# Kernel optimization log

Hardware: AMD Instinct MI355X
Metric: run time of the kernel (lower is better)

The kernel has to match this reference:

```python
import jax, jax.numpy as jnp
import numpy as np

D = 768
H = 12
HD = 64
S = 77
FF = 3072
EPS = 1e-5


def _layernorm(x, w, b):
    mu = jnp.mean(x, axis=-1, keepdims=True)
    var = jnp.mean(jnp.square(x - mu), axis=-1, keepdims=True)
    return (x - mu) * jax.lax.rsqrt(var + EPS) * w + b


def setup_inputs() -> dict:
    key = jax.random.key(0)
    ks = jax.random.split(key, 18)
    s = 1.0 / np.sqrt(D)
    sf = 1.0 / np.sqrt(FF)
    return {
        "x": jax.random.normal(ks[0], (512, S, D), dtype=jnp.float32),
        "ln1_w": jnp.ones((D,), jnp.float32),
        "ln1_b": jnp.zeros((D,), jnp.float32),
        "qw": jax.random.uniform(ks[1], (D, D), jnp.float32, -s, s),
        "qb": jax.random.uniform(ks[2], (D,), jnp.float32, -s, s),
        "kw": jax.random.uniform(ks[3], (D, D), jnp.float32, -s, s),
        "kb": jax.random.uniform(ks[4], (D,), jnp.float32, -s, s),
        "vw": jax.random.uniform(ks[5], (D, D), jnp.float32, -s, s),
        "vb": jax.random.uniform(ks[6], (D,), jnp.float32, -s, s),
        "ow": jax.random.uniform(ks[7], (D, D), jnp.float32, -s, s),
        "ob": jax.random.uniform(ks[8], (D,), jnp.float32, -s, s),
        "ln2_w": jnp.ones((D,), jnp.float32),
        "ln2_b": jnp.zeros((D,), jnp.float32),
        "fc1_w": jax.random.uniform(ks[9], (FF, D), jnp.float32, -s, s),
        "fc1_b": jax.random.uniform(ks[10], (FF,), jnp.float32, -s, s),
        "fc2_w": jax.random.uniform(ks[11], (D, FF), jnp.float32, -sf, sf),
        "fc2_b": jax.random.uniform(ks[12], (D,), jnp.float32, -sf, sf),
    }


def reference(x, ln1_w, ln1_b, qw, qb, kw, kb, vw, vb, ow, ob,
              ln2_w, ln2_b, fc1_w, fc1_b, fc2_w, fc2_b):
    B = x.shape[0]
    # --- attention block ---
    h = _layernorm(x, ln1_w, ln1_b)
    q = (h @ qw.T + qb) * 0.125
    k = h @ kw.T + kb
    v = h @ vw.T + vb
    # [B, S, H, HD] -> [B, H, S, HD]
    q = q.reshape(B, S, H, HD).transpose(0, 2, 1, 3)
    k = k.reshape(B, S, H, HD).transpose(0, 2, 1, 3)
    v = v.reshape(B, S, H, HD).transpose(0, 2, 1, 3)
    scores = jnp.einsum('bhqd,bhkd->bhqk', q, k)  # [B,H,S,S]
    # causal additive mask: -inf strictly above diagonal
    mask = jnp.triu(jnp.full((S, S), -jnp.inf, dtype=scores.dtype), 1)
    scores = scores + mask
    attn = jax.nn.softmax(scores, axis=-1)
    ctx = jnp.einsum('bhqk,bhkd->bhqd', attn, v)  # [B,H,S,HD]
    ctx = ctx.transpose(0, 2, 1, 3).reshape(B, S, D)
    x = x + (ctx @ ow.T + ob)
    # --- MLP block with QuickGELU ---
    res = x
    h2 = _layernorm(x, ln2_w, ln2_b) @ fc1_w.T + fc1_b
    h2 = h2 * jax.nn.sigmoid(h2 * 1.702)
    return res + (h2 @ fc2_w.T + fc2_b)
```

## Files before the change

kernel.cpp:

```cpp
#include <hip/hip_runtime.h>

typedef unsigned short u16;
typedef __bf16 v8bf __attribute__((ext_vector_type(8)));
typedef unsigned short u16x8 __attribute__((ext_vector_type(8)));
typedef float v4f __attribute__((ext_vector_type(4)));

#define DEV __device__ __forceinline__

constexpr int M_TOK = 512 * 77;

DEV u16 f2bf(float f) {
  union { float f; unsigned int u; } v; v.f = f;
  unsigned int r = v.u + 0x7fffu + ((v.u >> 16) & 1u);
  return (u16)(r >> 16);
}

DEV void gload16(const void* g, void* l) {
  __builtin_amdgcn_global_load_lds((const __attribute__((address_space(1))) void*)g,
                                   (__attribute__((address_space(3))) void*)l, 16, 0, 0);
}

__global__ void cvt4_k(const float* __restrict__ src, u16* __restrict__ dst, int n4, float scale) {
  int i = blockIdx.x * blockDim.x + threadIdx.x;
  if (i >= n4) return;
  const float4 v = ((const float4*)src)[i];
  ushort4 o;
  o.x = f2bf(v.x * scale); o.y = f2bf(v.y * scale);
  o.z = f2bf(v.z * scale); o.w = f2bf(v.w * scale);
  ((ushort4*)dst)[i] = o;
}

__global__ void qkvb_k(const float* __restrict__ qb, const float* __restrict__ kb,
                       const float* __restrict__ vb, float* __restrict__ dst) {
  int i = blockIdx.x * 256 + threadIdx.x;
  if (i >= 2304) return;
  dst[i] = (i < 768) ? qb[i] * 0.125f : (i < 1536 ? kb[i - 768] : vb[i - 1536]);
}

__global__ __launch_bounds__(256) void ln_k(const float* __restrict__ x, const float* __restrict__ w,
                                            const float* __restrict__ bvec, u16* __restrict__ out, int nrows) {
  const int lane = threadIdx.x & 63;
  const int row = blockIdx.x * 4 + (threadIdx.x >> 6);
  if (row >= nrows) return;
  const float4* xr = (const float4*)(x + (size_t)row * 768);
  float4 v[3];
  float sum = 0.f, sq = 0.f;
#pragma unroll
  for (int t = 0; t < 3; ++t) {
    v[t] = xr[lane + 64 * t];
    sum += v[t].x + v[t].y + v[t].z + v[t].w;
    sq  += v[t].x * v[t].x + v[t].y * v[t].y + v[t].z * v[t].z + v[t].w * v[t].w;
  }
#pragma unroll
  for (int o = 1; o < 64; o <<= 1) { sum += __shfl_xor(sum, o, 64); sq += __shfl_xor(sq, o, 64); }
  const float mean = sum * (1.f / 768.f);
  const float inv = rsqrtf(sq * (1.f / 768.f) - mean * mean + 1e-5f);
  u16* orow = out + (size_t)row * 768;
#pragma unroll
  for (int t = 0; t < 3; ++t) {
    const int c = 4 * (lane + 64 * t);
    ushort4 o4;
    o4.x = f2bf((v[t].x - mean) * inv * w[c + 0] + bvec[c + 0]);
    o4.y = f2bf((v[t].y - mean) * inv * w[c + 1] + bvec[c + 1]);
    o4.z = f2bf((v[t].z - mean) * inv * w[c + 2] + bvec[c + 2]);
    o4.w = f2bf((v[t].w - mean) * inv * w[c + 3] + bvec[c + 3]);
    *(ushort4*)(orow + c) = o4;
  }
}

template <int OUTF32, int ACT, int RES>
__global__ __launch_bounds__(256, 2) void gemm_k(
    const u16* __restrict__ A, const u16* __restrict__ Bw,
    const float* __restrict__ bias, const float* __restrict__ res,
    void* __restrict__ out, int M, int N, int K) {
  __shared__ u16 sA[2][128 * 32];
  __shared__ u16 sB[2][128 * 32];
  const int tid = threadIdx.x;
  const int lane = tid & 63;
  const int wv = tid >> 6;
  const int wr = wv >> 1, wc = wv & 1;
  const int m0 = blockIdx.y * 128, n0 = blockIdx.x * 128;
  const int frow = lane & 15, fk = (lane >> 4) * 8;

  v4f acc[4][4];
#pragma unroll
  for (int i = 0; i < 4; ++i)
#pragma unroll
    for (int j = 0; j < 4; ++j) acc[i][j] = (v4f){0.f, 0.f, 0.f, 0.f};

  const int srow = tid >> 2;
  const int skc = (tid & 3) * 8;
  const size_t aBase0 = (size_t)(m0 + srow) * K + skc;
  const size_t aBase1 = (size_t)(m0 + 64 + srow) * K + skc;
  const size_t bBase0 = (size_t)(n0 + srow) * K + skc;
  const size_t bBase1 = (size_t)(n0 + 64 + srow) * K + skc;
  const int ldsOff0 = (tid & ~63) * 8;

  auto stage = [&](int buf, int kt) {
    const int kb = kt * 32;
    gload16(A + aBase0 + kb, &sA[buf][ldsOff0]);
    gload16(A + aBase1 + kb, &sA[buf][2048 + ldsOff0]);
    gload16(Bw + bBase0 + kb, &sB[buf][ldsOff0]);
    gload16(Bw + bBase1 + kb, &sB[buf][2048 + ldsOff0]);
  };

  const int KT = K >> 5;
  stage(0, 0);
  __syncthreads();
  for (int kt = 0; kt < KT; ++kt) {
    const int cur = kt & 1;
    if (kt + 1 < KT) stage(cur ^ 1, kt + 1);
    v8bf fa[4], fb[4];
#pragma unroll
    for (int i = 0; i < 4; ++i)
      fa[i] = *(const v8bf*)&sA[cur][(wr * 64 + i * 16 + frow) * 32 + fk];
#pragma unroll
    for (int j = 0; j < 4; ++j)
      fb[j] = *(const v8bf*)&sB[cur][(wc * 64 + j * 16 + frow) * 32 + fk];
#pragma unroll
    for (int i = 0; i < 4; ++i)
#pragma unroll
      for (int j = 0; j < 4; ++j)
        acc[i][j] = __builtin_amdgcn_mfma_f32_16x16x32_bf16(fa[i], fb[j], acc[i][j], 0, 0, 0);
    __syncthreads();
  }

#pragma unroll
  for (int i = 0; i < 4; ++i) {
    const int rowb = m0 + wr * 64 + i * 16 + (lane >> 4) * 4;
#pragma unroll
    for (int j = 0; j < 4; ++j) {
      const int col = n0 + wc * 64 + j * 16 + (lane & 15);
      const float bv = bias[col];
#pragma unroll
      for (int r = 0; r < 4; ++r) {
        float v = acc[i][j][r] + bv;
        if (ACT) v = v * (1.f / (1.f + __expf(-1.702f * v)));
        const size_t off = (size_t)(rowb + r) * N + col;
        if (RES) v += res[off];
        if (OUTF32) ((float*)out)[off] = v;
        else ((u16*)out)[off] = f2bf(v);
      }
    }
  }
}

__global__ __launch_bounds__(256) void attn_k(const u16* __restrict__ qkv, u16* __restrict__ ctx) {
  __shared__ u16 sQK[10240];
  __shared__ u16 sVt[64 * 120];
  __shared__ float sS[80][81];
  const int tid = threadIdx.x;
  const int lane = tid & 63;
  const int wv = tid >> 6;
  const int b = blockIdx.x / 12;
  const int h = blockIdx.x % 12;
  u16* sQ = sQK;
  u16* sK = sQK + 5120;
  u16* sP = sQK;

  for (int i = tid; i < 10240 + 64 * 120; i += 256) {
    if (i < 10240) sQK[i] = 0; else sVt[i - 10240] = 0;
  }
  __syncthreads();

  const size_t tokBase = (size_t)(b * 77) * 2304 + h * 64;
  for (int c = tid; c < 77 * 8; c += 256) {
    const int row = c >> 3, k8 = (c & 7) * 8;
    const size_t src = tokBase + (size_t)row * 2304 + k8;
    *(u16x8*)&sQ[row * 64 + k8] = *(const u16x8*)&qkv[src];
    *(u16x8*)&sK[row * 64 + k8] = *(const u16x8*)&qkv[src + 768];
    u16x8 v = *(const u16x8*)&qkv[src + 1536];
#pragma unroll
    for (int j = 0; j < 8; ++j) sVt[(k8 + j) * 120 + row] = v[j];
  }
  __syncthreads();

  const int frow = lane & 15, fk = (lane >> 4) * 8;
  for (int t = wv; t < 25; t += 4) {
    const int it = t / 5, jt = t % 5;
    v4f acc = {0.f, 0.f, 0.f, 0.f};
#pragma unroll
    for (int kk = 0; kk < 2; ++kk) {
      v8bf a = *(const v8bf*)&sQ[(it * 16 + frow) * 64 + kk * 32 + fk];
      v8bf bb = *(const v8bf*)&sK[(jt * 16 + frow) * 64 + kk * 32 + fk];
      acc = __builtin_amdgcn_mfma_f32_16x16x32_bf16(a, bb, acc, 0, 0, 0);
    }
    const int col = jt * 16 + frow;
#pragma unroll
    for (int r = 0; r < 4; ++r) {
      const int row = it * 16 + (lane >> 4) * 4 + r;
      sS[row][col] = (col > row) ? -1e30f : acc[r];
    }
  }
  __syncthreads();

  if (tid < 80) {
    const int row = tid;
    float mx = -1e30f;
    for (int c2 = 0; c2 < 80; ++c2) mx = fmaxf(mx, sS[row][c2]);
    float sum = 0.f;
    for (int c2 = 0; c2 < 80; ++c2) { float e = __expf(sS[row][c2] - mx); sum += e; sS[row][c2] = e; }
    const float inv = 1.f / sum;
    for (int c2 = 0; c2 < 80; ++c2) sP[row * 96 + c2] = f2bf(sS[row][c2] * inv);
    for (int c2 = 80; c2 < 96; ++c2) sP[row * 96 + c2] = 0;
  }
  __syncthreads();

  const size_t outBase = (size_t)(b * 77) * 768 + h * 64;
  for (int t = wv; t < 20; t += 4) {
    const int it = t / 4, jt = t % 4;
    v4f acc = {0.f, 0.f, 0.f, 0.f};
#pragma unroll
    for (int kk = 0; kk < 3; ++kk) {
      v8bf a = *(const v8bf*)&sP[(it * 16 + frow) * 96 + kk * 32 + fk];
      v8bf bb = *(const v8bf*)&sVt[(jt * 16 + frow) * 120 + kk * 32 + fk];
      acc = __builtin_amdgcn_mfma_f32_16x16x32_bf16(a, bb, acc, 0, 0, 0);
    }
    const int col = jt * 16 + frow;
#pragma unroll
    for (int r = 0; r < 4; ++r) {
      const int row = it * 16 + (lane >> 4) * 4 + r;
      if (row < 77) ctx[outBase + (size_t)row * 768 + col] = f2bf(acc[r]);
    }
  }
}

extern "C" void kernel_launch(void* const* d_in, const int* in_sizes, int n_in,
                              void* d_out, int out_size, void* d_ws, size_t ws_size,
                              hipStream_t stream) {
  const float* x    = (const float*)d_in[0];
  const float* ln1w = (const float*)d_in[1];
  const float* ln1b = (const float*)d_in[2];
  const float* qw   = (const float*)d_in[3];
  const float* qb   = (const float*)d_in[4];
  const float* kw   = (const float*)d_in[5];
  const float* kb   = (const float*)d_in[6];
  const float* vw   = (const float*)d_in[7];
  const float* vb   = (const float*)d_in[8];
  const float* ow   = (const float*)d_in[9];
  const float* ob   = (const float*)d_in[10];
  const float* ln2w = (const float*)d_in[11];
  const float* ln2b = (const float*)d_in[12];
  const float* f1wf = (const float*)d_in[13];
  const float* f1b  = (const float*)d_in[14];
  const float* f2wf = (const float*)d_in[15];
  const float* f2b  = (const float*)d_in[16];
  float* outp = (float*)d_out;

  char* p = (char*)d_ws;
  auto alloc = [&](size_t bytes) { char* r = p; p += (bytes + 255) & ~(size_t)255; return r; };
  u16* wqkv = (u16*)alloc((size_t)2304 * 768 * 2);
  u16* owb  = (u16*)alloc((size_t)768 * 768 * 2);
  u16* f1w  = (u16*)alloc((size_t)3072 * 768 * 2);
  u16* f2w  = (u16*)alloc((size_t)768 * 3072 * 2);
  float* qkvb = (float*)alloc(2304 * 4);
  u16* bufA = (u16*)alloc((size_t)M_TOK * 768 * 2);
  u16* bufB = (u16*)alloc((size_t)M_TOK * 3072 * 2);

  cvt4_k<<<576, 256, 0, stream>>>(qw, wqkv, 147456, 0.125f);
  cvt4_k<<<576, 256, 0, stream>>>(kw, wqkv + 589824, 147456, 1.f);
  cvt4_k<<<576, 256, 0, stream>>>(vw, wqkv + 1179648, 147456, 1.f);
  cvt4_k<<<576, 256, 0, stream>>>(ow, owb, 147456, 1.f);
  cvt4_k<<<2304, 256, 0, stream>>>(f1wf, f1w, 589824, 1.f);
  cvt4_k<<<2304, 256, 0, stream>>>(f2wf, f2w, 589824, 1.f);
  qkvb_k<<<9, 256, 0, stream>>>(qb, kb, vb, qkvb);

  ln_k<<<M_TOK / 4, 256, 0, stream>>>(x, ln1w, ln1b, bufA, M_TOK);
  gemm_k<0, 0, 0><<<dim3(18, 308), 256, 0, stream>>>(bufA, wqkv, qkvb, nullptr, bufB, M_TOK, 2304, 768);
  attn_k<<<512 * 12, 256, 0, stream>>>(bufB, bufA);
  gemm_k<1, 0, 1><<<dim3(6, 308), 256, 0, stream>>>(bufA, owb, ob, x, outp, M_TOK, 768, 768);
  ln_k<<<M_TOK / 4, 256, 0, stream>>>(outp, ln2w, ln2b, bufA, M_TOK);
  gemm_k<0, 1, 0><<<dim3(24, 308), 256, 0, stream>>>(bufA, f1w, f1b, nullptr, bufB, M_TOK, 3072, 768);
  gemm_k<1, 0, 1><<<dim3(6, 308), 256, 0, stream>>>(bufB, f2w, f2b, outp, outp, M_TOK, 768, 3072);
}
```

Before: 1.083 ms.

## Replace 128x128 GEMM with 256x256 8-wave tile, 4-stage pipeline, XCD swizzle

Replaces the 128x128, 4-wave, double-buffered GEMM with a 256x256 tile run by 8 waves. It adds a 4-deep global-to-LDS pipeline with explicit vmcnt waits and barriers, an XOR-swizzled LDS layout to avoid bank conflicts, s_setprio around the MFMA bursts, and a workgroup remap that groups tiles per XCD for L2 locality. The goal is higher arithmetic intensity, fewer stalls on global loads, and better cache reuse. The costs are heavier register and LDS use (128KB of LDS per block), far fewer blocks, and dependence on M and N dividing by 256, which holds here (39424 = 154*256).

```diff
diff --git a/kernel.cpp b/kernel.cpp
--- a/kernel.cpp
+++ b/kernel.cpp
@@ -18,6 +18,10 @@
 DEV void gload16(const void* g, void* l) {
   __builtin_amdgcn_global_load_lds((const __attribute__((address_space(1))) void*)g,
                                    (__attribute__((address_space(3))) void*)l, 16, 0, 0);
+}
+
+DEV v4f MF(v8bf a, v8bf b, v4f c) {
+  return __builtin_amdgcn_mfma_f32_16x16x32_bf16(a, b, c, 0, 0, 0);
 }
 
 __global__ void cvt4_k(const float* __restrict__ src, u16* __restrict__ dst, int n4, float scale) {
@@ -69,74 +73,122 @@
 }
 
 template <int OUTF32, int ACT, int RES>
-__global__ __launch_bounds__(256, 2) void gemm_k(
+__global__ __launch_bounds__(512, 2) void gemm256_k(
     const u16* __restrict__ A, const u16* __restrict__ Bw,
     const float* __restrict__ bias, const float* __restrict__ res,
-    void* __restrict__ out, int M, int N, int K) {
-  __shared__ u16 sA[2][128 * 32];
-  __shared__ u16 sB[2][128 * 32];
+    void* __restrict__ out, int M, int N, int K, int nbx) {
+  __shared__ u16 lds[65536];
   const int tid = threadIdx.x;
   const int lane = tid & 63;
   const int wv = tid >> 6;
-  const int wr = wv >> 1, wc = wv & 1;
-  const int m0 = blockIdx.y * 128, n0 = blockIdx.x * 128;
-  const int frow = lane & 15, fk = (lane >> 4) * 8;
-
-  v4f acc[4][4];
-#pragma unroll
-  for (int i = 0; i < 4; ++i)
+  const int wr = wv >> 2, wc = wv & 3;
+
+  const int nwg = gridDim.x;
+  const int q = nwg >> 3, r8 = nwg & 7;
+  const int xcd = blockIdx.x & 7, cidx = blockIdx.x >> 3;
+  const int wg = (xcd < r8 ? xcd * (q + 1) : r8 * (q + 1) + (xcd - r8) * q) + cidx;
+  const int m0 = (wg / nbx) * 256;
+  const int n0 = (wg % nbx) * 256;
+
+  const int frow = lane & 15;
+  const int fq = lane >> 4;
+  const int chunkp = (fq ^ (lane & 3) ^ ((lane >> 2) & 3)) & 3;
+  const int aRd = (wr * 128 + frow) * 32 + chunkp * 8;
+  const int bRd = (wc * 64 + frow) * 32 + chunkp * 8;
+
+  const int srow = tid >> 2;
+  const int scg = ((tid & 3) ^ (srow & 3) ^ ((srow >> 2) & 3)) & 3;
+  const size_t aBase = (size_t)(m0 + srow) * K + scg * 8;
+  const size_t bBase = (size_t)(n0 + srow) * K + scg * 8;
+  const int ldsW = wv * 512;
+
+#define GLDA(kt, g) gload16(A + aBase + (size_t)(g) * 128 * K + (kt) * 32, \
+                            &lds[(((kt) & 3) << 14) + ((g) << 12) + ldsW])
+#define GLDB(kt, g) gload16(Bw + bBase + (size_t)(g) * 128 * K + (kt) * 32, \
+                            &lds[(((kt) & 3) << 14) + 8192 + ((g) << 12) + ldsW])
+#define BAR() asm volatile("s_barrier" ::: "memory")
+
+  v4f acc[8][4];
+#pragma unroll
+  for (int i = 0; i < 8; ++i)
 #pragma unroll
     for (int j = 0; j < 4; ++j) acc[i][j] = (v4f){0.f, 0.f, 0.f, 0.f};
 
-  const int srow = tid >> 2;
-  const int skc = (tid & 3) * 8;
-  const size_t aBase0 = (size_t)(m0 + srow) * K + skc;
-  const size_t aBase1 = (size_t)(m0 + 64 + srow) * K + skc;
-  const size_t bBase0 = (size_t)(n0 + srow) * K + skc;
-  const size_t bBase1 = (size_t)(n0 + 64 + srow) * K + skc;
-  const int ldsOff0 = (tid & ~63) * 8;
-
-  auto stage = [&](int buf, int kt) {
-    const int kb = kt * 32;
-    gload16(A + aBase0 + kb, &sA[buf][ldsOff0]);
-    gload16(A + aBase1 + kb, &sA[buf][2048 + ldsOff0]);
-    gload16(Bw + bBase0 + kb, &sB[buf][ldsOff0]);
-    gload16(Bw + bBase1 + kb, &sB[buf][2048 + ldsOff0]);
-  };
-
-  const int KT = K >> 5;
-  stage(0, 0);
-  __syncthreads();
-  for (int kt = 0; kt < KT; ++kt) {
-    const int cur = kt & 1;
-    if (kt + 1 < KT) stage(cur ^ 1, kt + 1);
-    v8bf fa[4], fb[4];
-#pragma unroll
-    for (int i = 0; i < 4; ++i)
-      fa[i] = *(const v8bf*)&sA[cur][(wr * 64 + i * 16 + frow) * 32 + fk];
-#pragma unroll
-    for (int j = 0; j < 4; ++j)
-      fb[j] = *(const v8bf*)&sB[cur][(wc * 64 + j * 16 + frow) * 32 + fk];
-#pragma unroll
-    for (int i = 0; i < 4; ++i)
-#pragma unroll
-      for (int j = 0; j < 4; ++j)
-        acc[i][j] = __builtin_amdgcn_mfma_f32_16x16x32_bf16(fa[i], fb[j], acc[i][j], 0, 0, 0);
-    __syncthreads();
-  }
-
-#pragma unroll
-  for (int i = 0; i < 4; ++i) {
-    const int rowb = m0 + wr * 64 + i * 16 + (lane >> 4) * 4;
+  const int NT = K >> 5;
+
+  GLDA(0, 0); GLDA(0, 1); GLDB(0, 0); GLDB(0, 1);
+  GLDA(1, 0); GLDA(1, 1); GLDB(1, 0); GLDB(1, 1);
+  GLDA(2, 0); GLDA(2, 1); GLDB(2, 0); GLDB(2, 1);
+  asm volatile("s_waitcnt vmcnt(8)" ::: "memory");
+  BAR();
+
+#define KTILE(kt, STG, VM)                                                      \
+  do {                                                                          \
+    const int sb = ((kt) & 3) << 14;                                            \
+    v8bf fa0 = *(const v8bf*)&lds[sb + aRd +    0];                             \
+    v8bf fa1 = *(const v8bf*)&lds[sb + aRd +  512];                             \
+    v8bf fa2 = *(const v8bf*)&lds[sb + aRd + 1024];                             \
+    v8bf fa3 = *(const v8bf*)&lds[sb + aRd + 1536];                             \
+    v8bf fb0 = *(const v8bf*)&lds[sb + 8192 + bRd +    0];                      \
+    v8bf fb1 = *(const v8bf*)&lds[sb + 8192 + bRd +  512];                      \
+    v8bf fb2 = *(const v8bf*)&lds[sb + 8192 + bRd + 1024];                      \
+    v8bf fb3 = *(const v8bf*)&lds[sb + 8192 + bRd + 1536];                      \
+    if (STG) { GLDA((kt) + 3, 0); GLDA((kt) + 3, 1); }                          \
+    BAR();                                                                      \
+    __builtin_amdgcn_s_setprio(1);                                              \
+    acc[0][0] = MF(fa0, fb0, acc[0][0]); acc[0][1] = MF(fa0, fb1, acc[0][1]);   \
+    acc[0][2] = MF(fa0, fb2, acc[0][2]); acc[0][3] = MF(fa0, fb3, acc[0][3]);   \
+    acc[1][0] = MF(fa1, fb0, acc[1][0]); acc[1][1] = MF(fa1, fb1, acc[1][1]);   \
+    acc[1][2] = MF(fa1, fb2, acc[1][2]); acc[1][3] = MF(fa1, fb3, acc[1][3]);   \
+    acc[2][0] = MF(fa2, fb0, acc[2][0]); acc[2][1] = MF(fa2, fb1, acc[2][1]);   \
+    acc[2][2] = MF(fa2, fb2, acc[2][2]); acc[2][3] = MF(fa2, fb3, acc[2][3]);   \
+    acc[3][0] = MF(fa3, fb0, acc[3][0]); acc[3][1] = MF(fa3, fb1, acc[3][1]);   \
+    acc[3][2] = MF(fa3, fb2, acc[3][2]); acc[3][3] = MF(fa3, fb3, acc[3][3]);   \
+    __builtin_amdgcn_s_setprio(0);                                              \
+    BAR();                                                                      \
+    v8bf fa4 = *(const v8bf*)&lds[sb + aRd + 2048];                             \
+    v8bf fa5 = *(const v8bf*)&lds[sb + aRd + 2560];                             \
+    v8bf fa6 = *(const v8bf*)&lds[sb + aRd + 3072];                             \
+    v8bf fa7 = *(const v8bf*)&lds[sb + aRd + 3584];                             \
+    if (STG) { GLDB((kt) + 3, 0); GLDB((kt) + 3, 1); }                          \
+    if ((VM) == 8) asm volatile("s_waitcnt vmcnt(8)" ::: "memory");             \
+    else if ((VM) == 4) asm volatile("s_waitcnt vmcnt(4)" ::: "memory");        \
+    else if ((VM) == 0) asm volatile("s_waitcnt vmcnt(0)" ::: "memory");        \
+    BAR();                                                                      \
+    __builtin_amdgcn_s_setprio(1);                                              \
+    acc[4][0] = MF(fa4, fb0, acc[4][0]); acc[4][1] = MF(fa4, fb1, acc[4][1]);   \
+    acc[4][2] = MF(fa4, fb2, acc[4][2]); acc[4][3] = MF(fa4, fb3, acc[4][3]);   \
+    acc[5][0] = MF(fa5, fb0, acc[5][0]); acc[5][1] = MF(fa5, fb1, acc[5][1]);   \
+    acc[5][2] = MF(fa5, fb2, acc[5][2]); acc[5][3] = MF(fa5, fb3, acc[5][3]);   \
+    acc[6][0] = MF(fa6, fb0, acc[6][0]); acc[6][1] = MF(fa6, fb1, acc[6][1]);   \
+    acc[6][2] = MF(fa6, fb2, acc[6][2]); acc[6][3] = MF(fa6, fb3, acc[6][3]);   \
+    acc[7][0] = MF(fa7, fb0, acc[7][0]); acc[7][1] = MF(fa7, fb1, acc[7][1]);   \
+    acc[7][2] = MF(fa7, fb2, acc[7][2]); acc[7][3] = MF(fa7, fb3, acc[7][3]);   \
+    __builtin_amdgcn_s_setprio(0);                                              \
+    BAR();                                                                      \
+  } while (0)
+
+  for (int kt = 0; kt + 3 < NT; ++kt) KTILE(kt, 1, 8);
+  KTILE(NT - 3, 0, 4);
+  KTILE(NT - 2, 0, 0);
+  KTILE(NT - 1, 0, -1);
+#undef KTILE
+#undef GLDA
+#undef GLDB
+#undef BAR
+
+#pragma unroll
+  for (int i = 0; i < 8; ++i) {
+    const int rowb = m0 + wr * 128 + i * 16 + fq * 4;
 #pragma unroll
     for (int j = 0; j < 4; ++j) {
-      const int col = n0 + wc * 64 + j * 16 + (lane & 15);
+      const int col = n0 + wc * 64 + j * 16 + frow;
       const float bv = bias[col];
 #pragma unroll
-      for (int r = 0; r < 4; ++r) {
-        float v = acc[i][j][r] + bv;
+      for (int rr = 0; rr < 4; ++rr) {
+        float v = acc[i][j][rr] + bv;
         if (ACT) v = v * (1.f / (1.f + __expf(-1.702f * v)));
-        const size_t off = (size_t)(rowb + r) * N + col;
+        const size_t off = (size_t)(rowb + rr) * N + col;
         if (RES) v += res[off];
         if (OUTF32) ((float*)out)[off] = v;
         else ((u16*)out)[off] = f2bf(v);
@@ -183,7 +235,7 @@
     for (int kk = 0; kk < 2; ++kk) {
       v8bf a = *(const v8bf*)&sQ[(it * 16 + frow) * 64 + kk * 32 + fk];
       v8bf bb = *(const v8bf*)&sK[(jt * 16 + frow) * 64 + kk * 32 + fk];
-      acc = __builtin_amdgcn_mfma_f32_16x16x32_bf16(a, bb, acc, 0, 0, 0);
+      acc = MF(a, bb, acc);
     }
     const int col = jt * 16 + frow;
 #pragma unroll
@@ -214,7 +266,7 @@
     for (int kk = 0; kk < 3; ++kk) {
       v8bf a = *(const v8bf*)&sP[(it * 16 + frow) * 96 + kk * 32 + fk];
       v8bf bb = *(const v8bf*)&sVt[(jt * 16 + frow) * 120 + kk * 32 + fk];
-      acc = __builtin_amdgcn_mfma_f32_16x16x32_bf16(a, bb, acc, 0, 0, 0);
+      acc = MF(a, bb, acc);
     }
     const int col = jt * 16 + frow;
 #pragma unroll
@@ -266,10 +318,10 @@
   qkvb_k<<<9, 256, 0, stream>>>(qb, kb, vb, qkvb);
 
   ln_k<<<M_TOK / 4, 256, 0, stream>>>(x, ln1w, ln1b, bufA, M_TOK);
-  gemm_k<0, 0, 0><<<dim3(18, 308), 256, 0, stream>>>(bufA, wqkv, qkvb, nullptr, bufB, M_TOK, 2304, 768);
+  gemm256_k<0, 0, 0><<<154 * 9, 512, 0, stream>>>(bufA, wqkv, qkvb, nullptr, bufB, M_TOK, 2304, 768, 9);
   attn_k<<<512 * 12, 256, 0, stream>>>(bufB, bufA);
-  gemm_k<1, 0, 1><<<dim3(6, 308), 256, 0, stream>>>(bufA, owb, ob, x, outp, M_TOK, 768, 768);
+  gemm256_k<1, 0, 1><<<154 * 3, 512, 0, stream>>>(bufA, owb, ob, x, outp, M_TOK, 768, 768, 3);
   ln_k<<<M_TOK / 4, 256, 0, stream>>>(outp, ln2w, ln2b, bufA, M_TOK);
-  gemm_k<0, 1, 0><<<dim3(24, 308), 256, 0, stream>>>(bufA, f1w, f1b, nullptr, bufB, M_TOK, 3072, 768);
-  gemm_k<1, 0, 1><<<dim3(6, 308), 256, 0, stream>>>(bufB, f2w, f2b, outp, outp, M_TOK, 768, 3072);
-}
+  gemm256_k<0, 1, 0><<<154 * 12, 512, 0, stream>>>(bufA, f1w, f1b, nullptr, bufB, M_TOK, 3072, 768, 12);
+  gemm256_k<1, 0, 1><<<154 * 3, 512, 0, stream>>>(bufB, f2w, f2b, outp, outp, M_TOK, 768, 3072, 3);
+}
```

Result: faster. 976.4 us (-9.9%).
